# Kernel tuning notes

Measured on AMD Instinct MI355X. Metric: run time of the kernel, lower is better.

The kernel has to match this reference:

```python
import jax, jax.numpy as jnp
import numpy as np

B, H, W = 8, 64, 64
D_MODEL = 256
NUM_FREQS = 10
MLP_WIDTH = 256
N = 16384
IN_DIM = 2 + 4 * NUM_FREQS + 3 * D_MODEL  # enc(42) + 3 pyramid levels * d_model


def _dense_params(key, din, dout):
    kw, kb = jax.random.split(key)
    w = jax.random.normal(kw, (din, dout), jnp.float32) / np.sqrt(din)
    b = jnp.zeros((dout,), jnp.float32)
    return w, b


def setup_inputs() -> dict:
    key = jax.random.key(0)
    ks = jax.random.split(key, 8)
    feature_grid = jax.random.normal(ks[0], (B, H, W, D_MODEL), jnp.float32)
    coords = jax.random.uniform(ks[1], (N, 2), jnp.float32) * 2.0 - 1.0  # in [-1, 1]
    w0, b0 = _dense_params(ks[2], IN_DIM, MLP_WIDTH)
    w1, b1 = _dense_params(ks[3], MLP_WIDTH, MLP_WIDTH)
    w2, b2 = _dense_params(ks[4], MLP_WIDTH, MLP_WIDTH)
    w3, b3 = _dense_params(ks[5], MLP_WIDTH + IN_DIM, MLP_WIDTH)  # skip concat before mlp_3
    w_out, b_out = _dense_params(ks[6], MLP_WIDTH, 3)
    return {"feature_grid": feature_grid, "coords": coords,
            "w0": w0, "b0": b0, "w1": w1, "b1": b1, "w2": w2, "b2": b2,
            "w3": w3, "b3": b3, "w_out": w_out, "b_out": b_out}


def _posenc(x):
    # [x, sin(x*f0), cos(x*f0), sin(x*f1), cos(x*f1), ...] along last axis
    freqs = 2.0 ** jnp.arange(NUM_FREQS, dtype=jnp.float32) * jnp.pi
    parts = [x]
    for f in freqs:
        parts.append(jnp.sin(x * f))
        parts.append(jnp.cos(x * f))
    return jnp.concatenate(parts, axis=-1)


def _sample_pyramid(feature_grid, coords):
    Bv, Hv, Wv, C = feature_grid.shape
    pyramid = [feature_grid] + [
        jax.image.resize(feature_grid, (Bv, Hv // 2 ** i, Wv // 2 ** i, C), 'bilinear')
        for i in range(1, 3)
    ]
    sampled = []
    for level_grid in pyramid:
        level_shape = jnp.array(level_grid.shape[1:3], dtype=jnp.float32)
        cr = (coords + 1.0) / 2.0 * (level_shape - 1.0)  # [N, 2] -> pixel coords

        def sample_one_image(g_hwc):
            g_chw = g_hwc.transpose(2, 0, 1)  # [C, h, w]
            samp = jax.vmap(lambda g: jax.scipy.ndimage.map_coordinates(
                g, cr.T, order=1, mode='reflect'))(g_chw)  # [C, N]
            return samp.T  # [N, C]

        sampled.append(jax.vmap(sample_one_image)(level_grid))  # [B, N, C]
    return jnp.concatenate(sampled, axis=-1)  # [B, N, 3C]


def reference(feature_grid, coords, w0, b0, w1, b1, w2, b2, w3, b3, w_out, b_out):
    Bv = feature_grid.shape[0]
    enc = _posenc(coords)  # [N, 42]
    feats = _sample_pyramid(feature_grid, coords)  # [B, N, 3*d_model]
    enc_tiled = jnp.broadcast_to(enc[None], (Bv,) + enc.shape)
    x = jnp.concatenate([enc_tiled, feats], axis=-1)  # [B, N, IN_DIM]
    h = jax.nn.gelu(x @ w0 + b0)
    h = jax.nn.gelu(h @ w1 + b1)
    h = jax.nn.gelu(h @ w2 + b2)
    h = jnp.concatenate([h, x], axis=-1)  # skip connection at depth//2
    h = jax.nn.gelu(h @ w3 + b3)
    return jnp.tanh(h @ w_out + b_out)  # [B, N, 3]
```

## Files before the change

### kernel.cpp

```cpp
#include <hip/hip_runtime.h>
#include <math.h>

#define BFULL 8
#define HH 64
#define WWI 64
#define CC 256
#define NN 16384
#define INDIM 810
#define XP 832
#define K3P 1088
#define MLPW 256
#define FBM 128
#define HSTR 264
#define ASTR 40

typedef unsigned short u16;
typedef __attribute__((ext_vector_type(8))) short short8;
typedef __attribute__((ext_vector_type(4))) float f32x4;

__device__ __forceinline__ u16 f2bf(float f){
  union{float f; unsigned u;} v; v.f=f;
  unsigned r = v.u + 0x7FFFu + ((v.u>>16)&1u);
  return (u16)(r>>16);
}
__device__ __forceinline__ float bf2f(u16 h){
  union{unsigned u; float f;} v; v.u = ((unsigned)h)<<16; return v.f;
}
__device__ __forceinline__ float gelu_fast(float x){
  float z = 0.7978845608028654f*(x + 0.044715f*x*x*x);
  float e = __expf(2.0f*z);
  float t = 1.0f - 2.0f/(e + 1.0f);
  return 0.5f*x*(1.0f+t);
}

template<int OUTD, int RR>
__global__ __launch_bounds__(256) void resize_kernel(const float* __restrict__ in,
                                                     float* __restrict__ out){
  int bidx = blockIdx.x;
  int ox = bidx % OUTD;
  int oy = (bidx / OUTD) % OUTD;
  int b  = bidx / (OUTD*OUTD);
  int c = threadIdx.x;

  float sy = (oy + 0.5f)*RR - 0.5f;
  float sx = (ox + 0.5f)*RR - 0.5f;
  int jy0 = (int)floorf(sy) - RR + 1;
  int jx0 = (int)floorf(sx) - RR + 1;

  float wy[2*RR], wx[2*RR];
  int   jys[2*RR], jxs[2*RR];
  int cy=0, cx=0; float sumy=0.f, sumx=0.f;
  #pragma unroll
  for(int t=0;t<2*RR;t++){
    int j = jy0 + t;
    if(j>=0 && j<HH){
      float w = 1.0f - fabsf((float)j - sy)/(float)RR;
      if(w > 0.f){ jys[cy]=j; wy[cy]=w; sumy+=w; cy++; }
    }
  }
  #pragma unroll
  for(int t=0;t<2*RR;t++){
    int j = jx0 + t;
    if(j>=0 && j<WWI){
      float w = 1.0f - fabsf((float)j - sx)/(float)RR;
      if(w > 0.f){ jxs[cx]=j; wx[cx]=w; sumx+=w; cx++; }
    }
  }
  float acc = 0.f;
  for(int i=0;i<cy;i++)
    for(int j=0;j<cx;j++)
      acc += wy[i]*wx[j]*in[(((size_t)b*HH + jys[i])*WWI + jxs[j])*CC + c];
  acc /= (sumy*sumx);
  out[(((size_t)b*OUTD + oy)*OUTD + ox)*CC + c] = acc;
}

__global__ __launch_bounds__(256) void sample_encode_v2(
    const float* __restrict__ fg, const float* __restrict__ pyr1,
    const float* __restrict__ pyr2, const float* __restrict__ coords,
    u16* __restrict__ X, int m0, int mcount){
  int mi = blockIdx.x*2 + (threadIdx.x >> 7);
  if(mi >= mcount) return;
  int u = threadIdx.x & 127;
  int m = m0 + mi;
  int b = m / NN;
  int n = m % NN;
  float c0 = coords[(size_t)n*2 + 0];
  float c1 = coords[(size_t)n*2 + 1];
  u16* xrow = X + (size_t)mi*XP;

  if(u >= 64){
    if(u < 106){
      int p = u - 64;
      float v;
      if(p < 2){ v = (p==0) ? c0 : c1; }
      else {
        int k = (p-2) >> 2;
        int r = (p-2) & 3;
        float f = (float)(1u<<k) * 3.14159265358979323846f;
        float a = (r & 1) ? c1 : c0;
        v = (r < 2) ? sinf(a*f) : cosf(a*f);
      }
      xrow[p] = f2bf(v);
    } else {
      xrow[INDIM + (u - 106)] = 0;
    }
    return;
  }

  int c4 = u*4;
  const float* grids[3];
  grids[0] = fg   + (size_t)b*HH*WWI*CC;
  grids[1] = pyr1 + (size_t)b*32*32*CC;
  grids[2] = pyr2 + (size_t)b*16*16*CC;
  const int dims[3] = {64, 32, 16};

  #pragma unroll
  for(int lvl=0; lvl<3; lvl++){
    int d = dims[lvl];
    float yy = (c0 + 1.0f)*0.5f*(float)(d-1);
    float xx = (c1 + 1.0f)*0.5f*(float)(d-1);
    yy = fminf(fmaxf(yy, 0.0f), (float)(d-1));
    xx = fminf(fmaxf(xx, 0.0f), (float)(d-1));
    int y0 = (int)yy, x0 = (int)xx;
    int y1 = min(y0+1, d-1), x1 = min(x0+1, d-1);
    float ty = yy - (float)y0, tx = xx - (float)x0;
    const float* g = grids[lvl];
    float4 v00 = *(const float4*)&g[((size_t)y0*d + x0)*CC + c4];
    float4 v01 = *(const float4*)&g[((size_t)y0*d + x1)*CC + c4];
    float4 v10 = *(const float4*)&g[((size_t)y1*d + x0)*CC + c4];
    float4 v11 = *(const float4*)&g[((size_t)y1*d + x1)*CC + c4];
    float w00 = (1.f-ty)*(1.f-tx), w01 = (1.f-ty)*tx, w10 = ty*(1.f-tx), w11 = ty*tx;
    float r0 = w00*v00.x + w01*v01.x + w10*v10.x + w11*v11.x;
    float r1 = w00*v00.y + w01*v01.y + w10*v10.y + w11*v11.y;
    float r2 = w00*v00.z + w01*v01.z + w10*v10.z + w11*v11.z;
    float r3 = w00*v00.w + w01*v01.w + w10*v10.w + w11*v11.w;
    unsigned lo = (unsigned)f2bf(r0) | ((unsigned)f2bf(r1) << 16);
    unsigned hi = (unsigned)f2bf(r2) | ((unsigned)f2bf(r3) << 16);
    unsigned* dst = (unsigned*)&xrow[42 + lvl*CC + c4];
    dst[0] = lo; dst[1] = hi;
  }
}

__global__ __launch_bounds__(256) void wconv(const float* __restrict__ W,
                                             u16* __restrict__ Wb, int K, int Kp){
  int idx = blockIdx.x*256 + threadIdx.x;
  if(idx >= 256*Kp) return;
  int n = idx / Kp, k = idx % Kp;
  float v = (k < K) ? W[(size_t)k*MLPW + n] : 0.f;
  Wb[idx] = f2bf(v);
}

__global__ __launch_bounds__(512, 4) void fused_mlp(
    const u16* __restrict__ X,
    const u16* __restrict__ wb0, const u16* __restrict__ wb1,
    const u16* __restrict__ wb2, const u16* __restrict__ wb3,
    const float* __restrict__ b0, const float* __restrict__ b1,
    const float* __restrict__ b2, const float* __restrict__ b3,
    const float* __restrict__ wo, const float* __restrict__ bo,
    float* __restrict__ out, int m0){
  __shared__ u16 Hs[FBM*HSTR];
  __shared__ u16 As[FBM*ASTR];

  int tid  = threadIdx.x;
  int lane = tid & 63, wv = tid >> 6;
  int wr = (wv>>2)*64, wc = (wv&3)*64;
  int rl = lane & 15, cl = lane & 15;
  int koffe = (lane >> 4)*8;
  int rg = (lane >> 4)*4;

  size_t gm = (size_t)blockIdx.x*FBM;

  f32x4 acc[4][4];
  #pragma unroll
  for(int i=0;i<4;i++)
    #pragma unroll
    for(int j=0;j<4;j++) acc[i][j] = (f32x4){0.f,0.f,0.f,0.f};

  int srow = tid >> 2, skp = tid & 3;
  auto stageX = [&](int xk){
    uint4 v = *(const uint4*)&X[(gm + srow)*XP + xk + skp*8];
    *(uint4*)&As[srow*ASTR + skp*8] = v;
  };
  auto mfma_chunk = [&](const u16* __restrict__ bw, int KpW, int gk,
                        const u16* __restrict__ aLDS, int astride, int ak){
    short8 af[4], bfr[4];
    #pragma unroll
    for(int f=0; f<4; f++)
      af[f] = *(const short8*)&aLDS[(wr + f*16 + rl)*astride + ak + koffe];
    #pragma unroll
    for(int f=0; f<4; f++)
      bfr[f] = *(const short8*)&bw[(size_t)(wc + f*16 + rl)*KpW + gk + koffe];
    #pragma unroll
    for(int i=0;i<4;i++)
      #pragma unroll
      for(int j=0;j<4;j++)
        acc[i][j] = __builtin_amdgcn_mfma_f32_16x16x32_bf16(af[i], bfr[j], acc[i][j], 0,0,0);
  };
  auto epilogue = [&](const float* __restrict__ bias){
    __syncthreads();
    #pragma unroll
    for(int j=0;j<4;j++){
      int ncol = wc + j*16 + cl;
      float bv = bias[ncol];
      #pragma unroll
      for(int i=0;i<4;i++)
        #pragma unroll
        for(int r=0;r<4;r++){
          int row = wr + i*16 + rg + r;
          Hs[row*HSTR + ncol] = f2bf(gelu_fast(acc[i][j][r] + bv));
        }
    }
    __syncthreads();
    #pragma unroll
    for(int i=0;i<4;i++)
      #pragma unroll
      for(int j=0;j<4;j++) acc[i][j] = (f32x4){0.f,0.f,0.f,0.f};
  };

  for(int kc=0; kc<XP/32; kc++){
    stageX(kc*32);
    __syncthreads();
    mfma_chunk(wb0, XP, kc*32, As, ASTR, 0);
    __syncthreads();
  }
  epilogue(b0);
  #pragma unroll 1
  for(int kc=0; kc<8; kc++) mfma_chunk(wb1, 256, kc*32, Hs, HSTR, kc*32);
  epilogue(b1);
  #pragma unroll 1
  for(int kc=0; kc<8; kc++) mfma_chunk(wb2, 256, kc*32, Hs, HSTR, kc*32);
  epilogue(b2);
  #pragma unroll 1
  for(int kc=0; kc<8; kc++) mfma_chunk(wb3, K3P, kc*32, Hs, HSTR, kc*32);
  for(int kc=8; kc<K3P/32; kc++){
    __syncthreads();
    stageX((kc-8)*32);
    __syncthreads();
    mfma_chunk(wb3, K3P, kc*32, As, ASTR, 0);
  }
  epilogue(b3);

  int orow = wv*16 + (lane >> 2);
  int kb = (lane & 3)*64;
  float p0=0.f, p1=0.f, p2=0.f;
  for(int i=0;i<64;i++){
    float hv = bf2f(Hs[orow*HSTR + kb + i]);
    const float* w = &wo[(size_t)(kb+i)*3];
    p0 += hv*w[0]; p1 += hv*w[1]; p2 += hv*w[2];
  }
  p0 += __shfl_xor(p0,1); p0 += __shfl_xor(p0,2);
  p1 += __shfl_xor(p1,1); p1 += __shfl_xor(p1,2);
  p2 += __shfl_xor(p2,1); p2 += __shfl_xor(p2,2);
  if((lane & 3) == 0){
    size_t gr = (size_t)m0 + gm + orow;
    out[gr*3+0] = tanhf(p0 + bo[0]);
    out[gr*3+1] = tanhf(p1 + bo[1]);
    out[gr*3+2] = tanhf(p2 + bo[2]);
  }
}

extern "C" void kernel_launch(void* const* d_in, const int* in_sizes, int n_in,
                              void* d_out, int out_size, void* d_ws, size_t ws_size,
                              hipStream_t stream){
  const float* fg     = (const float*)d_in[0];
  const float* coords = (const float*)d_in[1];
  const float* w0 = (const float*)d_in[2];  const float* b0 = (const float*)d_in[3];
  const float* w1 = (const float*)d_in[4];  const float* b1 = (const float*)d_in[5];
  const float* w2 = (const float*)d_in[6];  const float* b2 = (const float*)d_in[7];
  const float* w3 = (const float*)d_in[8];  const float* b3 = (const float*)d_in[9];
  const float* wo = (const float*)d_in[10]; const float* bo = (const float*)d_in[11];
  float* out = (float*)d_out;

  char* ws = (char*)d_ws;
  size_t off = 0;
  auto alloc = [&](size_t bytes)->void*{
    void* p = ws + off;
    off += (bytes + 255) & ~(size_t)255;
    return p;
  };
  auto rnd = [](size_t bytes)->size_t{ return (bytes + 255) & ~(size_t)255; };

  size_t fixed =
      rnd((size_t)BFULL*32*32*CC*4) + rnd((size_t)BFULL*16*16*CC*4) +
      rnd((size_t)256*XP*2) + rnd((size_t)256*256*2) +
      rnd((size_t)256*256*2) + rnd((size_t)256*K3P*2);

  const size_t Mtot = (size_t)BFULL*NN;
  size_t chunk = Mtot;
  while(chunk > 128){
    size_t need = fixed + rnd(chunk*(size_t)XP*2);
    if(need <= ws_size) break;
    chunk >>= 1;
  }
  size_t min_need = fixed + rnd(chunk*(size_t)XP*2);
  if(min_need > ws_size || (chunk % 128) != 0) return;

  float* pyr1 = (float*)alloc((size_t)BFULL*32*32*CC*4);
  float* pyr2 = (float*)alloc((size_t)BFULL*16*16*CC*4);
  u16* wb0 = (u16*)alloc((size_t)256*XP*2);
  u16* wb1 = (u16*)alloc((size_t)256*256*2);
  u16* wb2 = (u16*)alloc((size_t)256*256*2);
  u16* wb3 = (u16*)alloc((size_t)256*K3P*2);
  u16* X  = (u16*)alloc(chunk*(size_t)XP*2);

  resize_kernel<32,2><<<dim3(BFULL*32*32), dim3(256), 0, stream>>>(fg, pyr1);
  resize_kernel<16,4><<<dim3(BFULL*16*16), dim3(256), 0, stream>>>(fg, pyr2);
  wconv<<<dim3((256*XP +255)/256), dim3(256), 0, stream>>>(w0, wb0, INDIM, XP);
  wconv<<<dim3((256*256 +255)/256), dim3(256), 0, stream>>>(w1, wb1, 256, 256);
  wconv<<<dim3((256*256 +255)/256), dim3(256), 0, stream>>>(w2, wb2, 256, 256);
  wconv<<<dim3((256*K3P +255)/256), dim3(256), 0, stream>>>(w3, wb3, MLPW+INDIM, K3P);

  for(size_t m0=0; m0<Mtot; m0+=chunk){
    int mc = (int)chunk;
    sample_encode_v2<<<dim3(mc/2), dim3(256), 0, stream>>>(fg, pyr1, pyr2, coords, X, (int)m0, mc);
    fused_mlp<<<dim3(mc/FBM), dim3(512), 0, stream>>>(X, wb0, wb1, wb2, wb3,
                                                      b0, b1, b2, b3, wo, bo,
                                                      out, (int)m0);
  }
}
```

Baseline: 684.4 us.

## Prefetch X tiles into registers, unroll hidden loops, MFMA output layer

The X-staging loop now loads the next 32-column slice of X into registers while the current slice's MFMAs run, so global load latency is hidden behind compute. The hidden-layer loops are fully unrolled. The final 256->3 projection now runs on MFMA with a bf16 output weight padded to 16 columns, converted by a new small kernel, instead of a scalar FP32 dot-product loop. HSTR changes from 264 to 260 to alter LDS bank mapping. The output weights and hidden activations are now rounded to bf16 for the last layer, and the unrolled loops raise register pressure.

```diff
diff --git a/kernel.cpp b/kernel.cpp
--- a/kernel.cpp
+++ b/kernel.cpp
@@ -11,7 +11,7 @@
 #define K3P 1088
 #define MLPW 256
 #define FBM 128
-#define HSTR 264
+#define HSTR 260
 #define ASTR 40
 
 typedef unsigned short u16;
@@ -150,13 +150,23 @@
   Wb[idx] = f2bf(v);
 }
 
+__global__ __launch_bounds__(256) void wconv_out(const float* __restrict__ wo,
+                                                 u16* __restrict__ wob){
+  int idx = blockIdx.x*256 + threadIdx.x;
+  if(idx >= 16*256) return;
+  int n = idx >> 8, k = idx & 255;
+  float v = (n < 3) ? wo[(size_t)k*3 + n] : 0.f;
+  wob[idx] = f2bf(v);
+}
+
 __global__ __launch_bounds__(512, 4) void fused_mlp(
     const u16* __restrict__ X,
     const u16* __restrict__ wb0, const u16* __restrict__ wb1,
     const u16* __restrict__ wb2, const u16* __restrict__ wb3,
+    const u16* __restrict__ wob,
     const float* __restrict__ b0, const float* __restrict__ b1,
     const float* __restrict__ b2, const float* __restrict__ b3,
-    const float* __restrict__ wo, const float* __restrict__ bo,
+    const float* __restrict__ bo,
     float* __restrict__ out, int m0){
   __shared__ u16 Hs[FBM*HSTR];
   __shared__ u16 As[FBM*ASTR];
@@ -164,7 +174,7 @@
   int tid  = threadIdx.x;
   int lane = tid & 63, wv = tid >> 6;
   int wr = (wv>>2)*64, wc = (wv&3)*64;
-  int rl = lane & 15, cl = lane & 15;
+  int rl = lane & 15;
   int koffe = (lane >> 4)*8;
   int rg = (lane >> 4)*4;
 
@@ -177,30 +187,30 @@
     for(int j=0;j<4;j++) acc[i][j] = (f32x4){0.f,0.f,0.f,0.f};
 
   int srow = tid >> 2, skp = tid & 3;
-  auto stageX = [&](int xk){
-    uint4 v = *(const uint4*)&X[(gm + srow)*XP + xk + skp*8];
-    *(uint4*)&As[srow*ASTR + skp*8] = v;
-  };
-  auto mfma_chunk = [&](const u16* __restrict__ bw, int KpW, int gk,
-                        const u16* __restrict__ aLDS, int astride, int ak){
-    short8 af[4], bfr[4];
+  const u16* xbase = X + (gm + srow)*XP + skp*8;
+
+  auto loadA = [&](const u16* aL, int astr, int ak, short8 af[4]){
     #pragma unroll
     for(int f=0; f<4; f++)
-      af[f] = *(const short8*)&aLDS[(wr + f*16 + rl)*astride + ak + koffe];
+      af[f] = *(const short8*)&aL[(wr + f*16 + rl)*astr + ak + koffe];
+  };
+  auto loadB = [&](const u16* bw, int Kp2, int gk, short8 bf[4]){
     #pragma unroll
     for(int f=0; f<4; f++)
-      bfr[f] = *(const short8*)&bw[(size_t)(wc + f*16 + rl)*KpW + gk + koffe];
+      bf[f] = *(const short8*)&bw[(size_t)(wc + f*16 + rl)*Kp2 + gk + koffe];
+  };
+  auto domfma = [&](short8 af[4], short8 bf[4]){
     #pragma unroll
     for(int i=0;i<4;i++)
       #pragma unroll
       for(int j=0;j<4;j++)
-        acc[i][j] = __builtin_amdgcn_mfma_f32_16x16x32_bf16(af[i], bfr[j], acc[i][j], 0,0,0);
+        acc[i][j] = __builtin_amdgcn_mfma_f32_16x16x32_bf16(af[i], bf[j], acc[i][j], 0,0,0);
   };
   auto epilogue = [&](const float* __restrict__ bias){
     __syncthreads();
     #pragma unroll
     for(int j=0;j<4;j++){
-      int ncol = wc + j*16 + cl;
+      int ncol = wc + j*16 + rl;
       float bv = bias[ncol];
       #pragma unroll
       for(int i=0;i<4;i++)
@@ -216,46 +226,65 @@
       #pragma unroll
       for(int j=0;j<4;j++) acc[i][j] = (f32x4){0.f,0.f,0.f,0.f};
   };
-
-  for(int kc=0; kc<XP/32; kc++){
-    stageX(kc*32);
+  auto xloop = [&](const u16* bw, int Kp2, int gbase){
+    uint4 xv = *(const uint4*)(xbase);
+    *(uint4*)&As[srow*ASTR + skp*8] = xv;
     __syncthreads();
-    mfma_chunk(wb0, XP, kc*32, As, ASTR, 0);
-    __syncthreads();
-  }
+    for(int kc=0; kc<26; kc++){
+      uint4 xn;
+      if(kc < 25) xn = *(const uint4*)(xbase + (kc+1)*32);
+      short8 bf[4]; loadB(bw, Kp2, gbase + kc*32, bf);
+      short8 af[4]; loadA(As, ASTR, 0, af);
+      domfma(af, bf);
+      __syncthreads();
+      if(kc < 25) *(uint4*)&As[srow*ASTR + skp*8] = xn;
+      __syncthreads();
+    }
+  };
+  auto hloop = [&](const u16* bw, int Kp2, int gbase){
+    #pragma unroll
+    for(int kc=0; kc<8; kc++){
+      short8 bf[4]; loadB(bw, Kp2, gbase + kc*32, bf);
+      short8 af[4]; loadA(Hs, HSTR, kc*32, af);
+      domfma(af, bf);
+    }
+  };
+
+  xloop(wb0, XP, 0);
   epilogue(b0);
-  #pragma unroll 1
-  for(int kc=0; kc<8; kc++) mfma_chunk(wb1, 256, kc*32, Hs, HSTR, kc*32);
+  hloop(wb1, 256, 0);
   epilogue(b1);
-  #pragma unroll 1
-  for(int kc=0; kc<8; kc++) mfma_chunk(wb2, 256, kc*32, Hs, HSTR, kc*32);
+  hloop(wb2, 256, 0);
   epilogue(b2);
-  #pragma unroll 1
-  for(int kc=0; kc<8; kc++) mfma_chunk(wb3, K3P, kc*32, Hs, HSTR, kc*32);
-  for(int kc=8; kc<K3P/32; kc++){
-    __syncthreads();
-    stageX((kc-8)*32);
-    __syncthreads();
-    mfma_chunk(wb3, K3P, kc*32, As, ASTR, 0);
-  }
+  hloop(wb3, K3P, 0);
+  xloop(wb3, K3P, 256);
   epilogue(b3);
 
-  int orow = wv*16 + (lane >> 2);
-  int kb = (lane & 3)*64;
-  float p0=0.f, p1=0.f, p2=0.f;
-  for(int i=0;i<64;i++){
-    float hv = bf2f(Hs[orow*HSTR + kb + i]);
-    const float* w = &wo[(size_t)(kb+i)*3];
-    p0 += hv*w[0]; p1 += hv*w[1]; p2 += hv*w[2];
-  }
-  p0 += __shfl_xor(p0,1); p0 += __shfl_xor(p0,2);
-  p1 += __shfl_xor(p1,1); p1 += __shfl_xor(p1,2);
-  p2 += __shfl_xor(p2,1); p2 += __shfl_xor(p2,2);
-  if((lane & 3) == 0){
-    size_t gr = (size_t)m0 + gm + orow;
-    out[gr*3+0] = tanhf(p0 + bo[0]);
-    out[gr*3+1] = tanhf(p1 + bo[1]);
-    out[gr*3+2] = tanhf(p2 + bo[2]);
+  if(wv < 2){
+    f32x4 oa[4];
+    #pragma unroll
+    for(int i=0;i<4;i++) oa[i] = (f32x4){0.f,0.f,0.f,0.f};
+    #pragma unroll
+    for(int c=0;c<8;c++){
+      short8 af[4];
+      #pragma unroll
+      for(int f=0; f<4; f++)
+        af[f] = *(const short8*)&Hs[(wv*64 + f*16 + rl)*HSTR + c*32 + koffe];
+      short8 bf1 = *(const short8*)&wob[(size_t)rl*256 + c*32 + koffe];
+      #pragma unroll
+      for(int i=0;i<4;i++)
+        oa[i] = __builtin_amdgcn_mfma_f32_16x16x32_bf16(af[i], bf1, oa[i], 0,0,0);
+    }
+    if(rl < 3){
+      float bv = bo[rl];
+      #pragma unroll
+      for(int i=0;i<4;i++)
+        #pragma unroll
+        for(int r=0;r<4;r++){
+          size_t gr = (size_t)m0 + gm + wv*64 + i*16 + rg + r;
+          out[gr*3 + rl] = tanhf(oa[i][r] + bv);
+        }
+    }
   }
 }
 
@@ -283,7 +312,7 @@
   size_t fixed =
       rnd((size_t)BFULL*32*32*CC*4) + rnd((size_t)BFULL*16*16*CC*4) +
       rnd((size_t)256*XP*2) + rnd((size_t)256*256*2) +
-      rnd((size_t)256*256*2) + rnd((size_t)256*K3P*2);
+      rnd((size_t)256*256*2) + rnd((size_t)256*K3P*2) + rnd((size_t)16*256*2);
 
   const size_t Mtot = (size_t)BFULL*NN;
   size_t chunk = Mtot;
@@ -301,6 +330,7 @@
   u16* wb1 = (u16*)alloc((size_t)256*256*2);
   u16* wb2 = (u16*)alloc((size_t)256*256*2);
   u16* wb3 = (u16*)alloc((size_t)256*K3P*2);
+  u16* wob = (u16*)alloc((size_t)16*256*2);
   u16* X  = (u16*)alloc(chunk*(size_t)XP*2);
 
   resize_kernel<32,2><<<dim3(BFULL*32*32), dim3(256), 0, stream>>>(fg, pyr1);
@@ -309,12 +339,13 @@
   wconv<<<dim3((256*256 +255)/256), dim3(256), 0, stream>>>(w1, wb1, 256, 256);
   wconv<<<dim3((256*256 +255)/256), dim3(256), 0, stream>>>(w2, wb2, 256, 256);
   wconv<<<dim3((256*K3P +255)/256), dim3(256), 0, stream>>>(w3, wb3, MLPW+INDIM, K3P);
+  wconv_out<<<dim3(16), dim3(256), 0, stream>>>(wo, wob);
 
   for(size_t m0=0; m0<Mtot; m0+=chunk){
     int mc = (int)chunk;
     sample_encode_v2<<<dim3(mc/2), dim3(256), 0, stream>>>(fg, pyr1, pyr2, coords, X, (int)m0, mc);
-    fused_mlp<<<dim3(mc/FBM), dim3(512), 0, stream>>>(X, wb0, wb1, wb2, wb3,
-                                                      b0, b1, b2, b3, wo, bo,
+    fused_mlp<<<dim3(mc/FBM), dim3(512), 0, stream>>>(X, wb0, wb1, wb2, wb3, wob,
+                                                      b0, b1, b2, b3, bo,
                                                       out, (int)m0);
   }
 }
```

New measurement: 665.7 us. -2.7%, faster.
